# Kernel optimization log

Measured on AMD Instinct MI355X. Metric: run time of the kernel, lower is better.

The kernel has to match this reference:

```python
import jax, jax.numpy as jnp
import numpy as np

B, S, D, H = 4, 2048, 1024, 16
HD = D // H          # head_dim = 64; per-head scale = sqrt(HD) as in source
FF = 4096
EPS = 1e-5


def _layernorm(x, g, b):
    m = jnp.mean(x, axis=-1, keepdims=True)
    v = jnp.mean(jnp.square(x - m), axis=-1, keepdims=True)
    return (x - m) * jax.lax.rsqrt(v + EPS) * g + b


def setup_inputs() -> dict:
    key = jax.random.key(0)
    ks = jax.random.split(key, 10)
    std = 0.02
    return {
        "x": jax.random.normal(ks[0], (B, S, D), jnp.float32),
        "wq": jax.random.normal(ks[1], (H, D, HD), jnp.float32) * std,
        "bq": jnp.zeros((H, HD), jnp.float32),
        "wk": jax.random.normal(ks[2], (H, D, HD), jnp.float32) * std,
        "bk": jnp.zeros((H, HD), jnp.float32),
        "wv": jax.random.normal(ks[3], (H, D, HD), jnp.float32) * std,
        "bv": jnp.zeros((H, HD), jnp.float32),
        "wo": jax.random.normal(ks[4], (D, D), jnp.float32) * std,
        "bo": jnp.zeros((D,), jnp.float32),
        "w1": jax.random.normal(ks[5], (D, FF), jnp.float32) * std,
        "b1": jnp.zeros((FF,), jnp.float32),
        "w2": jax.random.normal(ks[6], (FF, D), jnp.float32) * std,
        "b2": jnp.zeros((D,), jnp.float32),
        "g1": jnp.ones((D,), jnp.float32),
        "beta1": jnp.zeros((D,), jnp.float32),
        "g2": jnp.ones((D,), jnp.float32),
        "beta2": jnp.zeros((D,), jnp.float32),
    }


def reference(x, wq, bq, wk, bk, wv, bv, wo, bo, w1, b1, w2, b2, g1, beta1, g2, beta2):
    # Per-head Q/K/V projections (stacked over heads) -> [B,H,S,HD]
    q = jnp.einsum('bsd,hdf->bhsf', x, wq) + bq[None, :, None, :]
    k = jnp.einsum('bsd,hdf->bhsf', x, wk) + bk[None, :, None, :]
    v = jnp.einsum('bsd,hdf->bhsf', x, wv) + bv[None, :, None, :]

    scale = jnp.sqrt(jnp.asarray(HD, jnp.float32))
    att = jnp.einsum('bhqf,bhkf->bhqk', q, k) / scale  # [B,H,S,S]
    causal = jnp.tril(jnp.ones((S, S), dtype=bool))
    att = jnp.where(causal[None, None], att, -jnp.inf)
    p = jax.nn.softmax(att, axis=-1)
    o = jnp.einsum('bhqk,bhkf->bhqf', p, v)            # [B,H,S,HD]
    o = o.transpose(0, 2, 1, 3).reshape(B, S, D)       # concat heads
    attn_out = o @ wo + bo

    h = _layernorm(x + attn_out, g1, beta1)            # post-LN, dropout=0 (eval)
    ff = jax.nn.gelu(h @ w1 + b1, approximate=False) @ w2 + b2
    return _layernorm(h + ff, g2, beta2)
```

## Files before the change

kernel.cpp:

```cpp
#include <hip/hip_runtime.h>
#include <hip/hip_bf16.h>
#include <math.h>

typedef __bf16 bf16x8 __attribute__((ext_vector_type(8)));
typedef float floatx4 __attribute__((ext_vector_type(4)));
typedef unsigned short ushort8 __attribute__((ext_vector_type(8)));
typedef unsigned short ushort4v __attribute__((ext_vector_type(4)));

__device__ __forceinline__ unsigned short f2bs(float f){
  union { float f; unsigned u; } v; v.f = f;
  unsigned r = v.u + 0x7fffu + ((v.u >> 16) & 1u);
  return (unsigned short)(r >> 16);
}
__device__ __forceinline__ float bs2f(unsigned short s){
  union { unsigned u; float f; } v; v.u = ((unsigned)s) << 16; return v.f;
}
__device__ __forceinline__ unsigned pk2(float a, float b){
  union { __hip_bfloat162 h; unsigned u; } cv;
  cv.h = __float22bfloat162_rn(make_float2(a, b));
  return cv.u;
}
__device__ __forceinline__ void gl_lds16(const void* g, void* l){
  __builtin_amdgcn_global_load_lds(
      (const __attribute__((address_space(1))) void*)g,
      (__attribute__((address_space(3))) void*)l,
      16, 0, 0);
}

__global__ __launch_bounds__(256) void prep(
    const float* __restrict__ x,  unsigned short* __restrict__ Xb,
    const float* __restrict__ wq, const float* __restrict__ wk,
    const float* __restrict__ wv, const float* __restrict__ bq,
    const float* __restrict__ bk, const float* __restrict__ bv,
    unsigned short* __restrict__ Wqkv, float* __restrict__ Bqkv,
    const float* __restrict__ wo, unsigned short* __restrict__ Wot,
    const float* __restrict__ w1, unsigned short* __restrict__ W1t,
    const float* __restrict__ w2, unsigned short* __restrict__ W2t){
  __shared__ float tile[32][65];
  const int blk = blockIdx.x, t = threadIdx.x;

  if (blk < 8192){
    const int i = (blk*256 + t)*4;
    const float4 v = *(const float4*)(x + i);
    ushort4v u = { f2bs(v.x), f2bs(v.y), f2bs(v.z), f2bs(v.w) };
    *(ushort4v*)(Xb + i) = u;
    return;
  }

  if (blk < 9728){
    const int p = blk - 8192;
    const int dt = p & 31, h = (p>>5)&15, sel = p>>9;
    const float* src = (sel==0 ? wq : (sel==1 ? wk : wv)) + (size_t)h*65536;
    const int d0 = dt*32;
    {
      const int r = t >> 3, cc = (t & 7)*8;
      const float* pp = src + (size_t)(d0+r)*64 + cc;
      const float4 v0 = *(const float4*)pp;
      const float4 v1 = *(const float4*)(pp+4);
      tile[r][cc+0]=v0.x; tile[r][cc+1]=v0.y; tile[r][cc+2]=v0.z; tile[r][cc+3]=v0.w;
      tile[r][cc+4]=v1.x; tile[r][cc+5]=v1.y; tile[r][cc+6]=v1.z; tile[r][cc+7]=v1.w;
    }
    __syncthreads();
    const int f = t >> 2, rr = (t & 3)*8;
    ushort8 u;
    #pragma unroll
    for (int j=0;j<8;j++) u[j] = f2bs(tile[rr+j][f]);
    const size_t n = (size_t)sel*1024 + h*64 + f;
    *(ushort8*)(Wqkv + n*1024 + d0 + rr) = u;
    if (dt==0 && t<64){
      const float* bs = (sel==0 ? bq : (sel==1 ? bk : bv)) + h*64;
      Bqkv[sel*1024 + h*64 + t] = bs[t];
    }
    return;
  }

  const float* src; unsigned short* dst; int R, C, bx, by;
  if (blk < 10240){ const int q = blk-9728;  src=wo; dst=Wot; R=1024; C=1024; bx=q&15; by=q>>4; }
  else if (blk < 12288){ const int q = blk-10240; src=w1; dst=W1t; R=1024; C=4096; bx=q&63; by=q>>6; }
  else { const int q = blk-12288; src=w2; dst=W2t; R=4096; C=1024; bx=q&15; by=q>>4; }
  const int r0 = by*32, c0 = bx*64;
  {
    const int r = t >> 3, cc = (t & 7)*8;
    const float* p = src + (size_t)(r0+r)*C + c0 + cc;
    const float4 v0 = *(const float4*)p;
    const float4 v1 = *(const float4*)(p+4);
    tile[r][cc+0]=v0.x; tile[r][cc+1]=v0.y; tile[r][cc+2]=v0.z; tile[r][cc+3]=v0.w;
    tile[r][cc+4]=v1.x; tile[r][cc+5]=v1.y; tile[r][cc+6]=v1.z; tile[r][cc+7]=v1.w;
  }
  __syncthreads();
  const int f = t >> 2, rr = (t & 3)*8;
  ushort8 u;
  #pragma unroll
  for (int j=0;j<8;j++) u[j] = f2bs(tile[rr+j][f]);
  *(ushort8*)(dst + (size_t)(c0+f)*R + r0 + rr) = u;
}

template<int MODE>
__global__ __launch_bounds__(256, 4)
void gemm_tn(const unsigned short* __restrict__ A,
             const unsigned short* __restrict__ Bt,
             const float* __restrict__ bias,
             void* __restrict__ out0,
             void* __restrict__ out1,
             void* __restrict__ out2,
             int K, int OW, int klen){
  __shared__ __align__(16) unsigned short As[128*32];
  __shared__ __align__(16) unsigned short Bs[128*32];
  const int tid = threadIdx.x;
  const int wave = tid >> 6, lane = tid & 63;
  const int quad = lane >> 4, l15 = lane & 15;
  const int lin = blockIdx.x;
  const int n0 = (lin & 63) << 7;
  const int m0 = (lin >> 6) << 7;
  const int kz = blockIdx.z;
  const int kbase = kz * klen;
  const int wr = (wave >> 1) << 6, wc = (wave & 1) << 6;

  floatx4 acc[4][4];
  #pragma unroll
  for (int i=0;i<4;i++)
    #pragma unroll
    for (int j=0;j<4;j++) acc[i][j] = (floatx4)0.0f;

  const unsigned short* gA[2];
  const unsigned short* gB[2];
  int lofs[2];
  #pragma unroll
  for (int r2=0;r2<2;r2++){
    const int slot = r2*256 + tid;
    const int rp = slot >> 3, rem = slot & 7;
    const int row = rp*2 + (rem >> 2);
    const int kc = (rem & 3) ^ (rp & 3);
    gA[r2] = A  + (size_t)(m0 + row)*K + kbase + kc*8;
    gB[r2] = Bt + (size_t)(n0 + row)*K + kbase + kc*8;
    lofs[r2] = slot*8;
  }
  int aofs[4], bofs[4];
  #pragma unroll
  for (int t=0;t<4;t++){
    const int ra = wr + t*16 + l15;
    aofs[t] = (ra>>1)*64 + (ra&1)*32 + ((quad ^ ((ra>>1)&3))<<3);
    const int rb = wc + t*16 + l15;
    bofs[t] = (rb>>1)*64 + (rb&1)*32 + ((quad ^ ((rb>>1)&3))<<3);
  }

  for (int k0 = 0; k0 < klen; k0 += 32){
    gl_lds16(gA[0] + k0, As + lofs[0]);
    gl_lds16(gA[1] + k0, As + lofs[1]);
    gl_lds16(gB[0] + k0, Bs + lofs[0]);
    gl_lds16(gB[1] + k0, Bs + lofs[1]);
    __syncthreads();
    bf16x8 af[4];
    #pragma unroll
    for (int t=0;t<4;t++) af[t] = *(const bf16x8*)(&As[aofs[t]]);
    #pragma unroll
    for (int j=0;j<4;j++){
      const bf16x8 bv = *(const bf16x8*)(&Bs[bofs[j]]);
      #pragma unroll
      for (int i=0;i<4;i++)
        acc[i][j] = __builtin_amdgcn_mfma_f32_16x16x32_bf16(af[i], bv, acc[i][j], 0,0,0);
    }
    __syncthreads();
  }

  #pragma unroll
  for (int i=0;i<4;i++){
    const int row0 = m0 + wr + i*16 + quad*4;
    float4 b4 = make_float4(0.f,0.f,0.f,0.f);
    if (MODE != 4 || kz == 0) b4 = *(const float4*)(bias + row0);
    #pragma unroll
    for (int j=0;j<4;j++){
      const int tok = n0 + wc + j*16 + l15;
      float v0 = acc[i][j][0] + b4.x;
      float v1 = acc[i][j][1] + b4.y;
      float v2 = acc[i][j][2] + b4.z;
      float v3 = acc[i][j][3] + b4.w;
      if (MODE == 1){
        float4 o4; o4.x=v0; o4.y=v1; o4.z=v2; o4.w=v3;
        *(float4*)((float*)out0 + (size_t)tok*OW + row0) = o4;
      } else if (MODE == 2){
        float vv[4] = {v0,v1,v2,v3};
        #pragma unroll
        for (int r=0;r<4;r++){
          const float v = vv[r];
          const float u = 0.7978845608f*v*(1.0f + 0.044715f*v*v);
          const float e = __builtin_amdgcn_exp2f(u * 2.885390082f);
          vv[r] = 0.5f*v*(1.0f + (1.0f - 2.0f/(1.0f + e)));
        }
        uint2 pkd = make_uint2(pk2(vv[0], vv[1]), pk2(vv[2], vv[3]));
        *(uint2*)((unsigned short*)out0 + (size_t)tok*4096 + row0) = pkd;
      } else if (MODE == 4){
        uint2 pkd = make_uint2(pk2(v0, v1), pk2(v2, v3));
        unsigned short* o = (unsigned short*)(kz ? out1 : out0);
        *(uint2*)(o + (size_t)tok*1024 + row0) = pkd;
      } else {
        if (row0 < 1024){
          const float s = 0.18033688011112042f;
          uint2 pkd = make_uint2(pk2(v0*s, v1*s), pk2(v2*s, v3*s));
          *(uint2*)((unsigned short*)out0 + (size_t)tok*1024 + row0) = pkd;
        } else if (row0 < 2048){
          uint2 pkd = make_uint2(pk2(v0, v1), pk2(v2, v3));
          *(uint2*)((unsigned short*)out1 + (size_t)tok*1024 + (row0-1024)) = pkd;
        } else {
          uint2 pkd = make_uint2(pk2(v0, v1), pk2(v2, v3));
          *(uint2*)((unsigned short*)out2 + (size_t)tok*1024 + (row0-2048)) = pkd;
        }
      }
    }
  }
}

#define VMCNT4 asm volatile("s_waitcnt vmcnt(4)" ::: "memory")
#define VMCNT0 asm volatile("s_waitcnt vmcnt(0)" ::: "memory")
#define TAILW { if (tg < NT-2) VMCNT4; else VMCNT0; }
#define LGKM4 { asm volatile("s_waitcnt lgkmcnt(4)" ::: "memory"); __builtin_amdgcn_sched_barrier(0); }
#define LGKM8 { asm volatile("s_waitcnt lgkmcnt(8)" ::: "memory"); __builtin_amdgcn_sched_barrier(0); }
#define LGKM0 { asm volatile("s_waitcnt lgkmcnt(0)" ::: "memory"); __builtin_amdgcn_sched_barrier(0); }

#define STAGE_A(T, H) { const int T_ = (T); if (T_ < NT){                     \
    unsigned short* l_ = lds + (T_&1)*32768 + (H)*8192;                       \
    const int ko_ = kbase + (T_<<6);                                          \
    gl_lds16(srcA##H##_0 + ko_, l_ + ch0*8);                                  \
    gl_lds16(srcA##H##_1 + ko_, l_ + ch1*8); } }
#define STAGE_B(T, H) { const int T_ = (T); if (T_ < NT){                     \
    unsigned short* l_ = lds + (T_&1)*32768 + 16384 + (H)*8192;               \
    const int ko_ = kbase + (T_<<6);                                          \
    gl_lds16(srcB##H##_0 + ko_, l_ + ch0*8);                                  \
    gl_lds16(srcB##H##_1 + ko_, l_ + ch1*8); } }

#define MFMA_Q(AF, BF, MH, NH)                                                \
    __builtin_amdgcn_s_setprio(1);                                            \
    _Pragma("unroll")                                                         \
    for (int k_=0;k_<2;k_++)                                                  \
      _Pragma("unroll")                                                       \
      for (int m_=0;m_<4;m_++)                                                \
        _Pragma("unroll")                                                     \
        for (int n_=0;n_<2;n_++)                                              \
          acc[(MH)*4+m_][(NH)*2+n_] = __builtin_amdgcn_mfma_f32_16x16x32_bf16( \
              AF[m_][k_], BF[n_][k_], acc[(MH)*4+m_][(NH)*2+n_], 0,0,0);      \
    __builtin_amdgcn_s_setprio(0);

#define RD_A(DST, BASE)                                                       \
    _Pragma("unroll")                                                         \
    for (int m_=0;m_<4;m_++)                                                  \
      _Pragma("unroll")                                                       \
      for (int k_=0;k_<2;k_++) DST[m_][k_] = *(const bf16x8*)((BASE) + aoff[m_][k_]);
#define RD_B(DST, BASE)                                                       \
    _Pragma("unroll")                                                         \
    for (int n_=0;n_<2;n_++)                                                  \
      _Pragma("unroll")                                                       \
      for (int k_=0;k_<2;k_++) DST[n_][k_] = *(const bf16x8*)((BASE) + boff[n_][k_]);

template<int MODE>
__global__ __launch_bounds__(512, 2)
void gemm256(const unsigned short* __restrict__ A,
             const unsigned short* __restrict__ Bt,
             const float* __restrict__ bias,
             void* __restrict__ out0,
             void* __restrict__ out1,
             void* __restrict__ out2,
             int K, int klen){
  __shared__ __align__(16) unsigned short lds[65536];
  const int tid = threadIdx.x;
  const int wave = tid >> 6, lane = tid & 63;
  const int quad = lane >> 4, l15 = lane & 15;
  const int wm = wave >> 2, wn = wave & 3;
  const int lin = blockIdx.x;
  const int n0 = (lin & 31) << 8;
  const int m0 = (lin >> 5) << 8;
  const int kz = blockIdx.z;
  const int kbase = kz * klen;
  const int NT = klen >> 6;

  const int r0 = tid >> 3;
  const int r1 = r0 + 64;
  const int g0 = (tid & 7) ^ (r0 & 7);
  const int ch0 = tid, ch1 = tid + 512;

  const unsigned short* srcA0_0 = A  + (size_t)(m0 +       r0)*K + g0*8;
  const unsigned short* srcA0_1 = A  + (size_t)(m0 +       r1)*K + g0*8;
  const unsigned short* srcA1_0 = A  + (size_t)(m0 + 128 + r0)*K + g0*8;
  const unsigned short* srcA1_1 = A  + (size_t)(m0 + 128 + r1)*K + g0*8;
  const unsigned short* srcB0_0 = Bt + (size_t)(n0 +       r0)*K + g0*8;
  const unsigned short* srcB0_1 = Bt + (size_t)(n0 +       r1)*K + g0*8;
  const unsigned short* srcB1_0 = Bt + (size_t)(n0 + 128 + r0)*K + g0*8;
  const unsigned short* srcB1_1 = Bt + (size_t)(n0 + 128 + r1)*K + g0*8;

  const int xr = l15 & 7;
  int aoff[4][2], boff[2][2];
  #pragma unroll
  for (int m=0;m<4;m++){
    const int rh = wm*64 + m*16 + l15;
    #pragma unroll
    for (int k=0;k<2;k++)
      aoff[m][k] = rh*64 + (((k*4 + quad) ^ xr) << 3);
  }
  #pragma unroll
  for (int n=0;n<2;n++){
    const int rb = wn*32 + n*16 + l15;
    #pragma unroll
    for (int k=0;k<2;k++)
      boff[n][k] = rb*64 + (((k*4 + quad) ^ xr) << 3);
  }

  floatx4 acc[8][4];
  #pragma unroll
  for (int i=0;i<8;i++)
    #pragma unroll
    for (int j=0;j<4;j++) acc[i][j] = (floatx4)0.0f;

  bf16x8 af0[4][2], af1[4][2], bf0[2][2], bf1[2][2];

  STAGE_B(0,0); STAGE_A(0,0); STAGE_A(0,1); STAGE_B(0,1);
  STAGE_B(1,0); STAGE_A(1,0);
  VMCNT4;
  __builtin_amdgcn_s_barrier();
  RD_A(af0, lds);
  RD_B(bf0, lds + 16384);

  for (int tg = 0; tg < NT; ++tg){
    const int d = tg & 1;
    const unsigned short* A1b = lds + d*32768 + 8192;
    const unsigned short* B1b = lds + d*32768 + 16384 + 8192;

    RD_B(bf1, B1b);
    STAGE_A(tg+1, 1);
    LGKM4;
    MFMA_Q(af0, bf0, 0, 0);

    RD_A(af1, A1b);
    STAGE_B(tg+1, 1);
    LGKM8;
    MFMA_Q(af0, bf1, 0, 1);
    __builtin_amdgcn_s_barrier();

    STAGE_B(tg+2, 0);
    LGKM0;
    MFMA_Q(af1, bf1, 1, 1);

    STAGE_A(tg+2, 0);
    TAILW;
    __builtin_amdgcn_s_barrier();
    {
      const unsigned short* A0n = lds + (d^1)*32768;
      const unsigned short* B0n = A0n + 16384;
      if (tg+1 < NT){ RD_A(af0, A0n); }
      MFMA_Q(af1, bf0, 1, 0);
      if (tg+1 < NT){ RD_B(bf0, B0n); }
    }
  }

  #pragma unroll
  for (int mh=0; mh<2; mh++){
    #pragma unroll
    for (int m=0; m<4; m++){
      const int row0 = m0 + mh*128 + wm*64 + m*16 + quad*4;
      float4 b4 = make_float4(0.f,0.f,0.f,0.f);
      if (MODE != 4 || kz == 0) b4 = *(const float4*)(bias + row0);
      #pragma unroll
      for (int nh=0; nh<2; nh++){
        #pragma unroll
        for (int n=0; n<2; n++){
          const int tok = n0 + nh*128 + wn*32 + n*16 + l15;
          const floatx4 a = acc[mh*4+m][nh*2+n];
          float v0 = a[0]+b4.x, v1 = a[1]+b4.y, v2 = a[2]+b4.z, v3 = a[3]+b4.w;
          if (MODE == 2){
            float vv[4] = {v0,v1,v2,v3};
            #pragma unroll
            for (int r=0;r<4;r++){
              const float v = vv[r];
              const float u = 0.7978845608f*v*(1.0f + 0.044715f*v*v);
              const float e = __builtin_amdgcn_exp2f(u * 2.885390082f);
              vv[r] = 0.5f*v*(1.0f + (1.0f - 2.0f/(1.0f + e)));
            }
            uint2 pkd = make_uint2(pk2(vv[0], vv[1]), pk2(vv[2], vv[3]));
            *(uint2*)((unsigned short*)out0 + (size_t)tok*4096 + row0) = pkd;
          } else if (MODE == 4){
            uint2 pkd = make_uint2(pk2(v0, v1), pk2(v2, v3));
            unsigned short* o = (unsigned short*)(kz ? out1 : out0);
            *(uint2*)(o + (size_t)tok*1024 + row0) = pkd;
          } else {
            if (row0 < 1024){
              const float s = 0.18033688011112042f;
              uint2 pkd = make_uint2(pk2(v0*s, v1*s), pk2(v2*s, v3*s));
              *(uint2*)((unsigned short*)out0 + (size_t)tok*1024 + row0) = pkd;
            } else if (row0 < 2048){
              uint2 pkd = make_uint2(pk2(v0, v1), pk2(v2, v3));
              *(uint2*)((unsigned short*)out1 + (size_t)tok*1024 + (row0-1024)) = pkd;
            } else {
              uint2 pkd = make_uint2(pk2(v0, v1), pk2(v2, v3));
              *(uint2*)((unsigned short*)out2 + (size_t)tok*1024 + (row0-2048)) = pkd;
            }
          }
        }
      }
    }
  }
}

__global__ __launch_bounds__(256) void vtrans(const unsigned short* __restrict__ Vtok,
                                              unsigned short* __restrict__ Vt){
  __shared__ unsigned short tile[64][65];
  const int st = blockIdx.x, bh = blockIdx.y;
  const int b = bh >> 4, h = bh & 15;
  const int t = threadIdx.x;
  {
    const int r = t >> 2, cc = (t & 3) * 16;
    const unsigned short* src = Vtok + (size_t)((b<<11) + (st<<6) + r)*1024 + (h<<6) + cc;
    ushort8 u0 = *(const ushort8*)src;
    ushort8 u1 = *(const ushort8*)(src + 8);
    #pragma unroll
    for (int j=0;j<8;j++){ tile[r][cc+j] = u0[j]; tile[r][cc+8+j] = u1[j]; }
  }
  __syncthreads();
  const int f = t >> 2, ss = (t & 3) * 16;
  ushort8 w0, w1;
  #pragma unroll
  for (int j=0;j<8;j++){ w0[j] = tile[ss+j][f]; w1[j] = tile[ss+8+j][f]; }
  unsigned short* dst = Vt + (size_t)bh*64*2048 + (size_t)f*2048 + (st<<6) + ss;
  *(ushort8*)dst = w0;
  *(ushort8*)(dst + 8) = w1;
}

__global__ __launch_bounds__(256, 4) void attn(const unsigned short* __restrict__ Q,
                                               const unsigned short* __restrict__ Kg,
                                               const unsigned short* __restrict__ Vt,
                                               unsigned short* __restrict__ O){
  __shared__ __align__(16) unsigned short Ks[64*64];
  __shared__ __align__(16) unsigned short Vs[64*64];
  __shared__ __align__(16) unsigned short PT[4][2][16*68];

  const int lin = blockIdx.x;
  const int bh = lin & 63;
  const int qt_lo = lin >> 6;
  const int qt_hi = 31 - qt_lo;
  const int b = bh >> 4, h = bh & 15;
  const int tid = threadIdx.x, wave = tid >> 6, lane = tid & 63;
  const int quad = lane >> 4, l15 = lane & 15;
  const float FM = 12.0f;

  const size_t qbase = (size_t)((b<<11) + (wave<<4) + l15)*1024 + (h<<6);
  bf16x8 qf_hi[2], qf_lo[2];
  qf_hi[0] = *(const bf16x8*)(Q + qbase + (size_t)(qt_hi<<6)*1024 + quad*8);
  qf_hi[1] = *(const bf16x8*)(Q + qbase + (size_t)(qt_hi<<6)*1024 + 32 + quad*8);
  qf_lo[0] = *(const bf16x8*)(Q + qbase + (size_t)(qt_lo<<6)*1024 + quad*8);
  qf_lo[1] = *(const bf16x8*)(Q + qbase + (size_t)(qt_lo<<6)*1024 + 32 + quad*8);

  floatx4 oa_hi[4], oa_lo[4];
  #pragma unroll
  for (int i=0;i<4;i++){ oa_hi[i] = (floatx4)0.0f; oa_lo[i] = (floatx4)0.0f; }
  float li_hi = 0.0f, li_lo = 0.0f;

  const unsigned short* Kbh = Kg + ((size_t)(b<<11))*1024 + (h<<6);
  const unsigned short* Vbh = Vt + (size_t)bh*64*2048;
  unsigned short* Pw0 = &PT[wave][0][0];
  unsigned short* Pw1 = &PT[wave][1][0];

  const int slot0 = wave*128 + lane;
  const int krow0 = slot0 >> 3, kc0 = (slot0 & 7) ^ (krow0 & 7);
  const int slot1 = slot0 + 64;
  const int krow1 = slot1 >> 3, kc1 = (slot1 & 7) ^ (krow1 & 7);

  auto softmax_P = [&](floatx4* sa, float& li, unsigned short* Pbuf, bool diag){
    if (diag){
      const int qrow = (wave<<4) + l15;
      #pragma unroll
      for (int tj=0;tj<4;tj++)
        #pragma unroll
        for (int r=0;r<4;r++)
          if (tj*16 + quad*4 + r > qrow) sa[tj][r] = -1e30f;
    }
    float rs = 0.0f;
    #pragma unroll
    for (int tj=0;tj<4;tj++)
      #pragma unroll
      for (int r=0;r<4;r++){
        const float p = __builtin_amdgcn_exp2f(sa[tj][r] - FM);
        sa[tj][r] = p;
        rs += p;
      }
    li += rs;
    #pragma unroll
    for (int tj=0;tj<4;tj++){
      uint2 pkd = make_uint2(pk2(sa[tj][0], sa[tj][1]), pk2(sa[tj][2], sa[tj][3]));
      *(uint2*)(Pbuf + l15*68 + tj*16 + quad*4) = pkd;
    }
  };

  for (int kt = 0; kt <= qt_hi; ++kt){
    gl_lds16(Kbh + (size_t)((kt<<6) + krow0)*1024 + kc0*8, Ks + wave*1024);
    gl_lds16(Kbh + (size_t)((kt<<6) + krow1)*1024 + kc1*8, Ks + wave*1024 + 512);
    gl_lds16(Vbh + (size_t)krow0*2048 + (kt<<6) + kc0*8, Vs + wave*1024);
    gl_lds16(Vbh + (size_t)krow1*2048 + (kt<<6) + kc1*8, Vs + wave*1024 + 512);
    __syncthreads();

    if (kt <= qt_lo){
      floatx4 sh[4], sl[4];
      __builtin_amdgcn_s_setprio(1);
      #pragma unroll
      for (int tj=0;tj<4;tj++){
        sh[tj] = (floatx4)0.0f; sl[tj] = (floatx4)0.0f;
        #pragma unroll
        for (int ks=0;ks<2;ks++){
          const int n = tj*16 + l15;
          const int c = (ks*4 + quad) ^ (n & 7);
          const bf16x8 kf = *(const bf16x8*)(Ks + n*64 + c*8);
          sh[tj] = __builtin_amdgcn_mfma_f32_16x16x32_bf16(kf, qf_hi[ks], sh[tj], 0,0,0);
          sl[tj] = __builtin_amdgcn_mfma_f32_16x16x32_bf16(kf, qf_lo[ks], sl[tj], 0,0,0);
        }
      }
      __builtin_amdgcn_s_setprio(0);
      softmax_P(sh, li_hi, Pw0, false);
      softmax_P(sl, li_lo, Pw1, kt == qt_lo);
      __builtin_amdgcn_s_setprio(1);
      #pragma unroll
      for (int ks2=0;ks2<2;ks2++){
        const bf16x8 pfh = *(const bf16x8*)(Pw0 + l15*68 + ks2*32 + quad*8);
        const bf16x8 pfl = *(const bf16x8*)(Pw1 + l15*68 + ks2*32 + quad*8);
        #pragma unroll
        for (int tn=0;tn<4;tn++){
          const int n2 = tn*16 + l15;
          const int c = (ks2*4 + quad) ^ (n2 & 7);
          const bf16x8 vf = *(const bf16x8*)(Vs + n2*64 + c*8);
          oa_hi[tn] = __builtin_amdgcn_mfma_f32_16x16x32_bf16(vf, pfh, oa_hi[tn], 0,0,0);
          oa_lo[tn] = __builtin_amdgcn_mfma_f32_16x16x32_bf16(vf, pfl, oa_lo[tn], 0,0,0);
        }
      }
      __builtin_amdgcn_s_setprio(0);
    } else {
      floatx4 sh[4];
      __builtin_amdgcn_s_setprio(1);
      #pragma unroll
      for (int tj=0;tj<4;tj++){
        sh[tj] = (floatx4)0.0f;
        #pragma unroll
        for (int ks=0;ks<2;ks++){
          const int n = tj*16 + l15;
          const int c = (ks*4 + quad) ^ (n & 7);
          const bf16x8 kf = *(const bf16x8*)(Ks + n*64 + c*8);
          sh[tj] = __builtin_amdgcn_mfma_f32_16x16x32_bf16(kf, qf_hi[ks], sh[tj], 0,0,0);
        }
      }
      __builtin_amdgcn_s_setprio(0);
      softmax_P(sh, li_hi, Pw0, kt == qt_hi);
      __builtin_amdgcn_s_setprio(1);
      #pragma unroll
      for (int ks2=0;ks2<2;ks2++){
        const bf16x8 pfh = *(const bf16x8*)(Pw0 + l15*68 + ks2*32 + quad*8);
        #pragma unroll
        for (int tn=0;tn<4;tn++){
          const int n2 = tn*16 + l15;
          const int c = (ks2*4 + quad) ^ (n2 & 7);
          const bf16x8 vf = *(const bf16x8*)(Vs + n2*64 + c*8);
          oa_hi[tn] = __builtin_amdgcn_mfma_f32_16x16x32_bf16(vf, pfh, oa_hi[tn], 0,0,0);
        }
      }
      __builtin_amdgcn_s_setprio(0);
    }
    __syncthreads();
  }

  li_hi += __shfl_xor(li_hi, 16, 64);
  li_hi += __shfl_xor(li_hi, 32, 64);
  li_lo += __shfl_xor(li_lo, 16, 64);
  li_lo += __shfl_xor(li_lo, 32, 64);
  {
    const float inv = 1.0f / li_hi;
    unsigned short* Orow = O + (size_t)((b<<11) + (qt_hi<<6) + (wave<<4) + l15)*1024 + (h<<6);
    #pragma unroll
    for (int tn=0;tn<4;tn++){
      uint2 pkd = make_uint2(pk2(oa_hi[tn][0]*inv, oa_hi[tn][1]*inv),
                             pk2(oa_hi[tn][2]*inv, oa_hi[tn][3]*inv));
      *(uint2*)(Orow + tn*16 + quad*4) = pkd;
    }
  }
  {
    const float inv = 1.0f / li_lo;
    unsigned short* Orow = O + (size_t)((b<<11) + (qt_lo<<6) + (wave<<4) + l15)*1024 + (h<<6);
    #pragma unroll
    for (int tn=0;tn<4;tn++){
      uint2 pkd = make_uint2(pk2(oa_lo[tn][0]*inv, oa_lo[tn][1]*inv),
                             pk2(oa_lo[tn][2]*inv, oa_lo[tn][3]*inv));
      *(uint2*)(Orow + tn*16 + quad*4) = pkd;
    }
  }
}

__global__ __launch_bounds__(256) void ln_res(const float* __restrict__ a,
                                              const float* __restrict__ bsrc,
                                              const float* __restrict__ g,
                                              const float* __restrict__ be,
                                              float* __restrict__ of,
                                              unsigned short* __restrict__ ob){
  __shared__ float red1[4], red2[4];
  const int row = blockIdx.x, t = threadIdx.x;
  const int wave = t >> 6, lane = t & 63;
  const float4 va = *(const float4*)(a + (size_t)row*1024 + t*4);
  const float4 vb = *(const float4*)(bsrc + (size_t)row*1024 + t*4);
  float xs[4] = {va.x+vb.x, va.y+vb.y, va.z+vb.z, va.w+vb.w};
  float s = xs[0]+xs[1]+xs[2]+xs[3];
  #pragma unroll
  for (int d=1; d<64; d<<=1) s += __shfl_xor(s, d, 64);
  if (lane==0) red1[wave] = s;
  __syncthreads();
  const float mean = (red1[0]+red1[1]+red1[2]+red1[3]) * (1.0f/1024.0f);
  float vsum = 0.0f;
  #pragma unroll
  for (int i=0;i<4;i++){ const float d = xs[i]-mean; vsum += d*d; }
  #pragma unroll
  for (int d=1; d<64; d<<=1) vsum += __shfl_xor(vsum, d, 64);
  if (lane==0) red2[wave] = vsum;
  __syncthreads();
  const float var = (red2[0]+red2[1]+red2[2]+red2[3]) * (1.0f/1024.0f);
  const float rs = rsqrtf(var + 1e-5f);
  const float4 gg = *(const float4*)(g + t*4);
  const float4 bb = *(const float4*)(be + t*4);
  float y[4];
  y[0] = (xs[0]-mean)*rs*gg.x + bb.x;
  y[1] = (xs[1]-mean)*rs*gg.y + bb.y;
  y[2] = (xs[2]-mean)*rs*gg.z + bb.z;
  y[3] = (xs[3]-mean)*rs*gg.w + bb.w;
  if (of){
    float4 o4; o4.x=y[0]; o4.y=y[1]; o4.z=y[2]; o4.w=y[3];
    *(float4*)(of + (size_t)row*1024 + t*4) = o4;
  }
  if (ob){
    ushort4v u = { f2bs(y[0]), f2bs(y[1]), f2bs(y[2]), f2bs(y[3]) };
    *(ushort4v*)(ob + (size_t)row*1024 + t*4) = u;
  }
}

__global__ __launch_bounds__(256) void ln_res2(const float* __restrict__ a,
                                               const unsigned short* __restrict__ p0,
                                               const unsigned short* __restrict__ p1,
                                               const float* __restrict__ g,
                                               const float* __restrict__ be,
                                               float* __restrict__ of){
  __shared__ float red1[4], red2[4];
  const int row = blockIdx.x, t = threadIdx.x;
  const int wave = t >> 6, lane = t & 63;
  const float4 va = *(const float4*)(a + (size_t)row*1024 + t*4);
  const ushort4v u0 = *(const ushort4v*)(p0 + (size_t)row*1024 + t*4);
  const ushort4v u1 = *(const ushort4v*)(p1 + (size_t)row*1024 + t*4);
  float xs[4] = { va.x + bs2f(u0[0]) + bs2f(u1[0]),
                  va.y + bs2f(u0[1]) + bs2f(u1[1]),
                  va.z + bs2f(u0[2]) + bs2f(u1[2]),
                  va.w + bs2f(u0[3]) + bs2f(u1[3]) };
  float s = xs[0]+xs[1]+xs[2]+xs[3];
  #pragma unroll
  for (int d=1; d<64; d<<=1) s += __shfl_xor(s, d, 64);
  if (lane==0) red1[wave] = s;
  __syncthreads();
  const float mean = (red1[0]+red1[1]+red1[2]+red1[3]) * (1.0f/1024.0f);
  float vsum = 0.0f;
  #pragma unroll
  for (int i=0;i<4;i++){ const float d = xs[i]-mean; vsum += d*d; }
  #pragma unroll
  for (int d=1; d<64; d<<=1) vsum += __shfl_xor(vsum, d, 64);
  if (lane==0) red2[wave] = vsum;
  __syncthreads();
  const float var = (red2[0]+red2[1]+red2[2]+red2[3]) * (1.0f/1024.0f);
  const float rs = rsqrtf(var + 1e-5f);
  const float4 gg = *(const float4*)(g + t*4);
  const float4 bb = *(const float4*)(be + t*4);
  float4 o4;
  o4.x = (xs[0]-mean)*rs*gg.x + bb.x;
  o4.y = (xs[1]-mean)*rs*gg.y + bb.y;
  o4.z = (xs[2]-mean)*rs*gg.z + bb.z;
  o4.w = (xs[3]-mean)*rs*gg.w + bb.w;
  *(float4*)(of + (size_t)row*1024 + t*4) = o4;
}

extern "C" void kernel_launch(void* const* d_in, const int* in_sizes, int n_in,
                              void* d_out, int out_size, void* d_ws, size_t ws_size,
                              hipStream_t stream){
  (void)in_sizes; (void)n_in; (void)out_size; (void)ws_size;
  const float* x  = (const float*)d_in[0];
  const float* wq = (const float*)d_in[1];
  const float* bq = (const float*)d_in[2];
  const float* wk = (const float*)d_in[3];
  const float* bk = (const float*)d_in[4];
  const float* wv = (const float*)d_in[5];
  const float* bv = (const float*)d_in[6];
  const float* wo = (const float*)d_in[7];
  const float* bo = (const float*)d_in[8];
  const float* w1 = (const float*)d_in[9];
  const float* b1 = (const float*)d_in[10];
  const float* w2 = (const float*)d_in[11];
  const float* b2 = (const float*)d_in[12];
  const float* g1 = (const float*)d_in[13];
  const float* be1= (const float*)d_in[14];
  const float* g2 = (const float*)d_in[15];
  const float* be2= (const float*)d_in[16];
  float* out = (float*)d_out;

  char* ws = (char*)d_ws;
  size_t off = 0;
  auto take = [&](size_t bytes)->char*{
    char* p = ws + off; off += (bytes + 255) & ~(size_t)255; return p;
  };
  unsigned short* Xb  = (unsigned short*)take(8192UL*1024*2);
  unsigned short* Qb  = (unsigned short*)take(8192UL*1024*2);
  unsigned short* Kb  = (unsigned short*)take(8192UL*1024*2);
  unsigned short* Vtb = (unsigned short*)take(8192UL*1024*2);
  unsigned short* Ob  = (unsigned short*)take(8192UL*1024*2);
  unsigned short* Midb= Qb;
  unsigned short* Vtok= (unsigned short*)take(8192UL*1024*2);
  unsigned short* Wqkv= (unsigned short*)take(3072UL*1024*2);
  float*          Bqkv= (float*)take(3072UL*4);
  unsigned short* Wot = (unsigned short*)take(1024UL*1024*2);
  unsigned short* W1t = (unsigned short*)take(4096UL*1024*2);
  unsigned short* W2t = (unsigned short*)take(1024UL*4096*2);
  float*          C1  = (float*)take(8192UL*1024*4);
  unsigned short* F0  = (unsigned short*)C1;
  unsigned short* F1  = F0 + 8192UL*1024;
  float*          Hf  = (float*)take(8192UL*1024*4);
  unsigned short* Hb  = (unsigned short*)take(8192UL*1024*2);

  prep<<<14336, 256, 0, stream>>>(x, Xb, wq, wk, wv, bq, bk, bv,
                                  Wqkv, Bqkv, wo, Wot, w1, W1t, w2, W2t);

  gemm256<3><<<12*32, 512, 0, stream>>>(Wqkv, Xb, Bqkv, Qb, Kb, Vtok, 1024, 1024);
  vtrans<<<dim3(32,64), 256, 0, stream>>>(Vtok, Vtb);

  attn<<<1024, 256, 0, stream>>>(Qb, Kb, Vtb, Ob);

  gemm_tn<1><<<8*64, 256, 0, stream>>>(Wot, Ob, bo, C1, nullptr, nullptr, 1024, 1024, 1024);
  ln_res<<<8192, 256, 0, stream>>>(x, C1, g1, be1, Hf, Hb);

  gemm256<2><<<16*32, 512, 0, stream>>>(W1t, Hb, b1, Midb, nullptr, nullptr, 1024, 1024);
  gemm256<4><<<dim3(4*32,1,2), 512, 0, stream>>>(W2t, Midb, b2, F0, F1, nullptr, 4096, 2048);
  ln_res2<<<8192, 256, 0, stream>>>(Hf, F0, F1, g2, be2, out);
}
```

Baseline: 500.4 us.

## Double-buffer K/V tiles in attention to prefetch the next tile during compute

The attention kernel now keeps two LDS buffers each for K and V. Right after the barrier it issues the async global-to-LDS load for the next key tile, so that load overlaps the MFMA and softmax work on the current tile. This also drops the trailing barrier at the end of each iteration. The extra 16 KB of LDS per block means the launch-bounds occupancy hint falls from 4 to 3 blocks per CU, which lowers the number of waves available to hide latency.

```diff
diff --git a/kernel.cpp b/kernel.cpp
--- a/kernel.cpp
+++ b/kernel.cpp
@@ -422,12 +422,12 @@
   *(ushort8*)(dst + 8) = w1;
 }
 
-__global__ __launch_bounds__(256, 4) void attn(const unsigned short* __restrict__ Q,
+__global__ __launch_bounds__(256, 3) void attn(const unsigned short* __restrict__ Q,
                                                const unsigned short* __restrict__ Kg,
                                                const unsigned short* __restrict__ Vt,
                                                unsigned short* __restrict__ O){
-  __shared__ __align__(16) unsigned short Ks[64*64];
-  __shared__ __align__(16) unsigned short Vs[64*64];
+  __shared__ __align__(16) unsigned short Ks[2*64*64];
+  __shared__ __align__(16) unsigned short Vs[2*64*64];
   __shared__ __align__(16) unsigned short PT[4][2][16*68];
 
   const int lin = blockIdx.x;
@@ -461,6 +461,15 @@
   const int slot1 = slot0 + 64;
   const int krow1 = slot1 >> 3, kc1 = (slot1 & 7) ^ (krow1 & 7);
 
+  auto stage_kv = [&](int kt, int dd){
+    unsigned short* Kd = Ks + dd*4096;
+    unsigned short* Vd = Vs + dd*4096;
+    gl_lds16(Kbh + (size_t)((kt<<6) + krow0)*1024 + kc0*8, Kd + wave*1024);
+    gl_lds16(Kbh + (size_t)((kt<<6) + krow1)*1024 + kc1*8, Kd + wave*1024 + 512);
+    gl_lds16(Vbh + (size_t)krow0*2048 + (kt<<6) + kc0*8, Vd + wave*1024);
+    gl_lds16(Vbh + (size_t)krow1*2048 + (kt<<6) + kc1*8, Vd + wave*1024 + 512);
+  };
+
   auto softmax_P = [&](floatx4* sa, float& li, unsigned short* Pbuf, bool diag){
     if (diag){
       const int qrow = (wave<<4) + l15;
@@ -487,12 +496,15 @@
     }
   };
 
+  stage_kv(0, 0);
+
   for (int kt = 0; kt <= qt_hi; ++kt){
-    gl_lds16(Kbh + (size_t)((kt<<6) + krow0)*1024 + kc0*8, Ks + wave*1024);
-    gl_lds16(Kbh + (size_t)((kt<<6) + krow1)*1024 + kc1*8, Ks + wave*1024 + 512);
-    gl_lds16(Vbh + (size_t)krow0*2048 + (kt<<6) + kc0*8, Vs + wave*1024);
-    gl_lds16(Vbh + (size_t)krow1*2048 + (kt<<6) + kc1*8, Vs + wave*1024 + 512);
+    const int d = kt & 1;
+    const unsigned short* Kd = Ks + d*4096;
+    const unsigned short* Vd = Vs + d*4096;
+
     __syncthreads();
+    if (kt < qt_hi) stage_kv(kt+1, d^1);
 
     if (kt <= qt_lo){
       floatx4 sh[4], sl[4];
@@ -504,7 +516,7 @@
         for (int ks=0;ks<2;ks++){
           const int n = tj*16 + l15;
           const int c = (ks*4 + quad) ^ (n & 7);
-          const bf16x8 kf = *(const bf16x8*)(Ks + n*64 + c*8);
+          const bf16x8 kf = *(const bf16x8*)(Kd + n*64 + c*8);
           sh[tj] = __builtin_amdgcn_mfma_f32_16x16x32_bf16(kf, qf_hi[ks], sh[tj], 0,0,0);
           sl[tj] = __builtin_amdgcn_mfma_f32_16x16x32_bf16(kf, qf_lo[ks], sl[tj], 0,0,0);
         }
@@ -521,7 +533,7 @@
         for (int tn=0;tn<4;tn++){
           const int n2 = tn*16 + l15;
           const int c = (ks2*4 + quad) ^ (n2 & 7);
-          const bf16x8 vf = *(const bf16x8*)(Vs + n2*64 + c*8);
+          const bf16x8 vf = *(const bf16x8*)(Vd + n2*64 + c*8);
           oa_hi[tn] = __builtin_amdgcn_mfma_f32_16x16x32_bf16(vf, pfh, oa_hi[tn], 0,0,0);
           oa_lo[tn] = __builtin_amdgcn_mfma_f32_16x16x32_bf16(vf, pfl, oa_lo[tn], 0,0,0);
         }
@@ -537,7 +549,7 @@
         for (int ks=0;ks<2;ks++){
           const int n = tj*16 + l15;
           const int c = (ks*4 + quad) ^ (n & 7);
-          const bf16x8 kf = *(const bf16x8*)(Ks + n*64 + c*8);
+          const bf16x8 kf = *(const bf16x8*)(Kd + n*64 + c*8);
           sh[tj] = __builtin_amdgcn_mfma_f32_16x16x32_bf16(kf, qf_hi[ks], sh[tj], 0,0,0);
         }
       }
@@ -551,13 +563,12 @@
         for (int tn=0;tn<4;tn++){
           const int n2 = tn*16 + l15;
           const int c = (ks2*4 + quad) ^ (n2 & 7);
-          const bf16x8 vf = *(const bf16x8*)(Vs + n2*64 + c*8);
+          const bf16x8 vf = *(const bf16x8*)(Vd + n2*64 + c*8);
           oa_hi[tn] = __builtin_amdgcn_mfma_f32_16x16x32_bf16(vf, pfh, oa_hi[tn], 0,0,0);
         }
       }
       __builtin_amdgcn_s_setprio(0);
     }
-    __syncthreads();
   }
 
   li_hi += __shfl_xor(li_hi, 16, 64);
```

New measurement: 518.5 us. 3.6% more time.
